# Performance work log

Hardware: AMD Instinct MI355X
Metric: run time of the kernel (lower is better)

The kernel has to match this reference:

```python
import jax, jax.numpy as jnp
import numpy as np

B, S, D, H = 2, 2048, 1024, 16
HD = D // H  # head_dim = 64


def setup_inputs() -> dict:
    key = jax.random.key(0)
    ks = jax.random.split(key, 10)
    sc = 1.0 / np.sqrt(D)
    x = jax.random.normal(ks[0], (B, S, D), dtype=jnp.float32)
    # causal mask, 0 = masked (module does masked_fill(mask == 0, -1e9))
    mask = jnp.broadcast_to(jnp.tril(jnp.ones((S, S), dtype=jnp.int32)), (B, S, S))
    return {
        "x": x,
        "mask": mask,
        "Wq": jax.random.normal(ks[1], (D, D), dtype=jnp.float32) * sc,
        "bq": jnp.zeros((D,), dtype=jnp.float32),
        "Wk": jax.random.normal(ks[2], (D, D), dtype=jnp.float32) * sc,
        "bk": jnp.zeros((D,), dtype=jnp.float32),
        "Wv": jax.random.normal(ks[3], (D, D), dtype=jnp.float32) * sc,
        "bv": jnp.zeros((D,), dtype=jnp.float32),
        "Wo": jax.random.normal(ks[4], (D, D), dtype=jnp.float32) * sc,
        "bo": jnp.zeros((D,), dtype=jnp.float32),
    }


def reference(x, mask, Wq, bq, Wk, bk, Wv, bv, Wo, bo):
    b, s, _ = x.shape
    # torch nn.Linear: y = x @ W.T + b
    def split_heads(t):
        return t.reshape(b, s, H, HD).transpose(0, 2, 1, 3)  # [B,H,S,hd]
    q = split_heads(x @ Wq.T + bq)
    k = split_heads(x @ Wk.T + bk)
    v = split_heads(x @ Wv.T + bv)
    scores = jnp.einsum("bhqd,bhkd->bhqk", q, k) / jnp.sqrt(jnp.float32(HD))
    scores = jnp.where(mask[:, None, :, :] == 0, jnp.float32(-1e9), scores)
    w = jax.nn.softmax(scores, axis=-1)
    out = jnp.einsum("bhqk,bhkd->bhqd", w, v)  # [B,H,S,hd]
    out = out.transpose(0, 2, 1, 3).reshape(b, s, D)
    return out @ Wo.T + bo
```

## Files before the change

kernel.cpp:

```cpp
#include <hip/hip_runtime.h>
#include <cstdint>


typedef __bf16 bf16x8 __attribute__((ext_vector_type(8)));
typedef float f32x4 __attribute__((ext_vector_type(4)));

__device__ inline f32x4 mfma16(bf16x8 a, bf16x8 b, f32x4 c) {
    return __builtin_amdgcn_mfma_f32_16x16x32_bf16(a, b, c, 0, 0, 0);
}

__device__ inline uint16_t f2bf(float f) {
    uint32_t u = __builtin_bit_cast(uint32_t, f);
    u += 0x7FFFu + ((u >> 16) & 1u);
    return (uint16_t)(u >> 16);
}

__device__ inline void gload_lds16(const uint16_t* g, uint16_t* l) {
    __builtin_amdgcn_global_load_lds(
        (const __attribute__((address_space(1))) uint32_t*)g,
        (__attribute__((address_space(3))) uint32_t*)l, 16, 0, 0);
}

__global__ __launch_bounds__(256) void cast_all(const float* __restrict__ x,
                                                const float* __restrict__ wq,
                                                const float* __restrict__ wk,
                                                const float* __restrict__ wv,
                                                const float* __restrict__ wo,
                                                uint16_t* __restrict__ xbf,
                                                uint16_t* __restrict__ wbf) {
    int i = blockIdx.x * 256 + threadIdx.x;
    float4 v;
    uint64_t* dp;
    if (i < (1 << 20)) {
        v = ((const float4*)x)[i];
        dp = (uint64_t*)xbf + i;
    } else {
        int j = i - (1 << 20);
        const float* ws[4] = {wq, wk, wv, wo};
        v = ((const float4*)ws[j >> 18])[j & 0x3FFFF];
        dp = (uint64_t*)wbf + j;
    }
    uint64_t p = (uint64_t)f2bf(v.x) | ((uint64_t)f2bf(v.y) << 16) |
                 ((uint64_t)f2bf(v.z) << 32) | ((uint64_t)f2bf(v.w) << 48);
    *dp = p;
}

template<int OUTF32, int BN>
__global__ __launch_bounds__(256) void gemm128(const uint16_t* __restrict__ A,
                                               const uint16_t* __restrict__ W,
                                               const float* __restrict__ b0,
                                               const float* __restrict__ b1,
                                               const float* __restrict__ b2,
                                               void* __restrict__ o0,
                                               void* __restrict__ o1,
                                               void* __restrict__ o2,
                                               int K, float s0, float s1, float s2) {
    constexpr int NT = BN / 32;
    __shared__ __align__(16) uint16_t SH[2 * (128 + BN) * 32];
    const int tid = threadIdx.x;
    const int lane = tid & 63, w = tid >> 6;
    const int l16 = lane & 15, quad = lane >> 4;
    const int wm = w & 1, wn = w >> 1;
    const int m0 = blockIdx.x * 128, n0 = blockIdx.y * BN;

    f32x4 acc[4][NT] = {};

    const int ci0 = w * 128 + lane;
    const uint16_t* ga0 = A + (size_t)(m0 + (ci0 >> 2)) * K + (ci0 & 3) * 8;
    const int ci1 = ci0 + 64;
    const uint16_t* ga1 = A + (size_t)(m0 + (ci1 >> 2)) * K + (ci1 & 3) * 8;
    const uint16_t* gb0 = W + (size_t)(n0 + (ci0 >> 2)) * K + (ci0 & 3) * 8;
    const uint16_t* gb1 = W + (size_t)(n0 + (ci1 >> 2)) * K + (ci1 & 3) * 8;
    const uint16_t* gbS = W + (size_t)(n0 + (tid >> 2)) * K + (tid & 3) * 8;

    uint16_t* A0 = SH;
    uint16_t* B0 = SH + 128 * 32;
    uint16_t* A1 = SH + (128 + BN) * 32;
    uint16_t* B1 = A1 + 128 * 32;

    gload_lds16(ga0, A0 + (w * 2 + 0) * 512);
    gload_lds16(ga1, A0 + (w * 2 + 1) * 512);
    if constexpr (BN == 128) {
        gload_lds16(gb0, B0 + (w * 2 + 0) * 512);
        gload_lds16(gb1, B0 + (w * 2 + 1) * 512);
    } else {
        gload_lds16(gbS, B0 + w * 512);
    }

    const int niter = K >> 5;
    for (int i = 0; i < niter; ++i) {
        __syncthreads();
        if (i + 1 < niter) {
            const int k1 = (i + 1) << 5;
            uint16_t* Ad = (i & 1) ? A0 : A1;
            uint16_t* Bd = (i & 1) ? B0 : B1;
            gload_lds16(ga0 + k1, Ad + (w * 2 + 0) * 512);
            gload_lds16(ga1 + k1, Ad + (w * 2 + 1) * 512);
            if constexpr (BN == 128) {
                gload_lds16(gb0 + k1, Bd + (w * 2 + 0) * 512);
                gload_lds16(gb1 + k1, Bd + (w * 2 + 1) * 512);
            } else {
                gload_lds16(gbS + k1, Bd + w * 512);
            }
        }
        const uint16_t* Ab = (i & 1) ? A1 : A0;
        const uint16_t* Bb = (i & 1) ? B1 : B0;
        bf16x8 af[4], bw[NT];
#pragma unroll
        for (int t = 0; t < 4; ++t)
            af[t] = *(const bf16x8*)(Ab + (wm * 64 + t * 16 + l16) * 32 + quad * 8);
#pragma unroll
        for (int t = 0; t < NT; ++t)
            bw[t] = *(const bf16x8*)(Bb + (wn * (BN / 2) + t * 16 + l16) * 32 + quad * 8);
#pragma unroll
        for (int mt = 0; mt < 4; ++mt)
#pragma unroll
            for (int nt = 0; nt < NT; ++nt)
                acc[mt][nt] = mfma16(af[mt], bw[nt], acc[mt][nt]);
    }

    const int seg = n0 >> 10, lc0 = n0 & 1023;
    const float* bp = (seg == 0) ? b0 : (seg == 1 ? b1 : b2);
    const float scale = (seg == 0) ? s0 : (seg == 1 ? s1 : s2);
    void* op = (seg == 0) ? o0 : (seg == 1 ? o1 : o2);

    if constexpr (OUTF32) {
#pragma unroll
        for (int nt = 0; nt < NT; ++nt) {
            int lcol = lc0 + wn * (BN / 2) + nt * 16 + l16;
            float bc = bp[lcol];
#pragma unroll
            for (int mt = 0; mt < 4; ++mt)
#pragma unroll
                for (int r = 0; r < 4; ++r) {
                    int row = m0 + wm * 64 + mt * 16 + quad * 4 + r;
                    ((float*)op)[(size_t)row * 1024 + lcol] = (acc[mt][nt][r] + bc) * scale;
                }
        }
    } else {
        __syncthreads();
        uint16_t* EP = SH;
#pragma unroll
        for (int nt = 0; nt < NT; ++nt) {
            float bc = bp[lc0 + wn * (BN / 2) + nt * 16 + l16];
#pragma unroll
            for (int mt = 0; mt < 4; ++mt)
#pragma unroll
                for (int r = 0; r < 4; ++r)
                    EP[(wm * 64 + mt * 16 + quad * 4 + r) * 128 +
                       wn * (BN / 2) + nt * 16 + l16] =
                        f2bf((acc[mt][nt][r] + bc) * scale);
        }
        __syncthreads();
        if (seg == 2) {
            const int bb = m0 >> 11, s0v = m0 & 2047;
            const int h0 = (n0 - 2048) >> 6;
            uint16_t* vtb = (uint16_t*)op + ((size_t)(bb * 16 + h0) * 64) * 2048 + s0v;
#pragma unroll
            for (int it = 0; it < 8; ++it) {
                int id = it * 256 + tid;
                int c = id & 127, sg = id >> 7;
                uint32_t wpk[4];
#pragma unroll
                for (int jj = 0; jj < 4; ++jj) {
                    uint32_t lo = EP[(sg * 8 + 2 * jj) * 128 + c];
                    uint32_t hi = EP[(sg * 8 + 2 * jj + 1) * 128 + c];
                    wpk[jj] = lo | (hi << 16);
                }
                uint4 o; o.x = wpk[0]; o.y = wpk[1]; o.z = wpk[2]; o.w = wpk[3];
                *(uint4*)(vtb + (size_t)c * 2048 + sg * 8) = o;
            }
        } else {
#pragma unroll
            for (int p = 0; p < 8; ++p) {
                int row = p * 16 + (tid >> 4);
                int c8 = (tid & 15) * 8;
                uint4 v = *(const uint4*)(EP + row * 128 + c8);
                *(uint4*)((uint16_t*)op + (size_t)(m0 + row) * 1024 + lc0 + c8) = v;
            }
        }
    }
}

__global__ __launch_bounds__(256) void attn_kernel(const uint16_t* __restrict__ Q,
                                                   const uint16_t* __restrict__ K,
                                                   const uint16_t* __restrict__ Vt,
                                                   uint16_t* __restrict__ att) {
    const int S = 2048, D = 1024;
    constexpr int LD = 72;
    __shared__ __align__(16) uint16_t Plds[4 * 32 * LD];

    const int bh = blockIdx.y;
    const int qb = (bh & 16) ? (int)blockIdx.x : 15 - (int)blockIdx.x;
    const int niter = 2 * qb + 2, kb_diag = 2 * qb;

    const int b = bh >> 4, h = bh & 15;
    const int tid = threadIdx.x, lane = tid & 63, w = tid >> 6;
    const int l16 = lane & 15, quad = lane >> 4;
    const int q0 = qb * 128;
    const size_t baseQK = (size_t)b * S * D + h * 64;
    uint16_t* Pw = Plds + w * (32 * LD);

    bf16x8 aq[2][2];
#pragma unroll
    for (int mt = 0; mt < 2; ++mt)
#pragma unroll
        for (int c = 0; c < 2; ++c)
            aq[mt][c] = *(const bf16x8*)(Q + baseQK +
                (size_t)(q0 + w * 32 + mt * 16 + l16) * D + c * 32 + quad * 8);

    bf16x8 ones;
#pragma unroll
    for (int j = 0; j < 8; ++j) ones[j] = (__bf16)1.0f;

    f32x4 accO[2][4] = {};
    f32x4 accL[2] = {};

    const uint16_t* Kf = K + baseQK + (size_t)l16 * D + quad * 8;
    const uint16_t* Vf = Vt + ((size_t)bh * 64 + l16) * S + quad * 8;

    for (int kb = 0; kb < niter; ++kb) {
        const uint16_t* Kt = Kf + (size_t)(kb * 64) * D;
        bf16x8 k0[4], k1[4];
#pragma unroll
        for (int t = 0; t < 4; ++t) {
            k0[t] = *(const bf16x8*)(Kt + (size_t)(t * 16) * D);
            k1[t] = *(const bf16x8*)(Kt + (size_t)(t * 16) * D + 32);
        }

        f32x4 sc[2][4];
#pragma unroll
        for (int t = 0; t < 4; ++t) {
            f32x4 z0 = {}; f32x4 z1 = {};
            sc[0][t] = mfma16(k1[t], aq[0][1], mfma16(k0[t], aq[0][0], z0));
            sc[1][t] = mfma16(k1[t], aq[1][1], mfma16(k0[t], aq[1][0], z1));
        }

        const uint16_t* Vtt = Vf + kb * 64;
        bf16x8 bv0[4], bv1[4];
#pragma unroll
        for (int nt = 0; nt < 4; ++nt) {
            bv0[nt] = *(const bf16x8*)(Vtt + (size_t)(nt * 16) * S);
            bv1[nt] = *(const bf16x8*)(Vtt + (size_t)(nt * 16) * S + 32);
        }

        if (kb < kb_diag) {
#pragma unroll
            for (int mt = 0; mt < 2; ++mt) {
                uint16_t* prow = Pw + (mt * 16 + l16) * LD + quad * 4;
#pragma unroll
                for (int t = 0; t < 4; ++t) {
                    uint64_t pk = 0;
#pragma unroll
                    for (int r = 0; r < 4; ++r) {
                        float p = __builtin_amdgcn_exp2f(sc[mt][t][r]);
                        pk |= (uint64_t)(uint16_t)(__builtin_bit_cast(uint32_t, p) >> 16)
                              << (16 * r);
                    }
                    *(uint64_t*)(prow + t * 16) = pk;
                }
            }
        } else {
#pragma unroll
            for (int mt = 0; mt < 2; ++mt) {
                const int qrow = q0 + w * 32 + mt * 16 + l16;
                uint16_t* prow = Pw + (mt * 16 + l16) * LD + quad * 4;
#pragma unroll
                for (int t = 0; t < 4; ++t) {
                    const int kc0 = kb * 64 + t * 16 + quad * 4;
                    uint64_t pk = 0;
#pragma unroll
                    for (int r = 0; r < 4; ++r) {
                        float s = sc[mt][t][r];
                        if (kc0 + r > qrow) s = -1e30f;
                        float p = __builtin_amdgcn_exp2f(s);
                        pk |= (uint64_t)(uint16_t)(__builtin_bit_cast(uint32_t, p) >> 16)
                              << (16 * r);
                    }
                    *(uint64_t*)(prow + t * 16) = pk;
                }
            }
        }

        __asm__ volatile("s_waitcnt lgkmcnt(0)" ::: "memory");

        bf16x8 ap0[2], ap1[2];
#pragma unroll
        for (int mt = 0; mt < 2; ++mt) {
            ap0[mt] = *(const bf16x8*)(Pw + (mt * 16 + l16) * LD + quad * 8);
            ap1[mt] = *(const bf16x8*)(Pw + (mt * 16 + l16) * LD + 32 + quad * 8);
        }
#pragma unroll
        for (int nt = 0; nt < 4; ++nt) {
            accO[0][nt] = mfma16(ap1[0], bv1[nt], mfma16(ap0[0], bv0[nt], accO[0][nt]));
            accO[1][nt] = mfma16(ap1[1], bv1[nt], mfma16(ap0[1], bv0[nt], accO[1][nt]));
        }
        accL[0] = mfma16(ap1[0], ones, mfma16(ap0[0], ones, accL[0]));
        accL[1] = mfma16(ap1[1], ones, mfma16(ap0[1], ones, accL[1]));
    }

    __asm__ volatile("s_waitcnt lgkmcnt(0)" ::: "memory");
#pragma unroll
    for (int mt = 0; mt < 2; ++mt)
#pragma unroll
        for (int r = 0; r < 4; ++r) {
            float inv = __builtin_amdgcn_rcpf(accL[mt][r]);
            const int rl = mt * 16 + quad * 4 + r;
#pragma unroll
            for (int nt = 0; nt < 4; ++nt)
                Pw[rl * LD + nt * 16 + l16] = f2bf(accO[mt][nt][r] * inv);
        }
    __asm__ volatile("s_waitcnt lgkmcnt(0)" ::: "memory");
#pragma unroll
    for (int p = 0; p < 4; ++p) {
        int row = p * 8 + (lane >> 3);
        int c8 = (lane & 7) * 8;
        uint4 v = *(const uint4*)(Pw + row * LD + c8);
        *(uint4*)(att + (size_t)(b * S + q0 + w * 32 + row) * 1024 + h * 64 + c8) = v;
    }
}

extern "C" void kernel_launch(void* const* d_in, const int* in_sizes, int n_in,
                              void* d_out, int out_size, void* d_ws, size_t ws_size,
                              hipStream_t stream) {
    const float* x  = (const float*)d_in[0];
    const float* Wq = (const float*)d_in[2];
    const float* bq = (const float*)d_in[3];
    const float* Wk = (const float*)d_in[4];
    const float* bk = (const float*)d_in[5];
    const float* Wv = (const float*)d_in[6];
    const float* bv = (const float*)d_in[7];
    const float* Wo = (const float*)d_in[8];
    const float* bo = (const float*)d_in[9];
    float* out = (float*)d_out;

    const int B = 2, S = 2048, D = 1024, H = 16;
    const int M = B * S;

    uint8_t* w = (uint8_t*)d_ws;
    uint16_t* xbf  = (uint16_t*)(w);
    uint16_t* wqbf = (uint16_t*)(w + (size_t)( 8 << 20));
    uint16_t* qbf  = (uint16_t*)(w + (size_t)(16 << 20));
    uint16_t* kbf  = (uint16_t*)(w + (size_t)(24 << 20));
    uint16_t* vtbf = (uint16_t*)(w + (size_t)(40 << 20));
    uint16_t* wobf = wqbf + (size_t)3 * D * D;
    uint16_t* attbf = xbf;

    cast_all<<<dim3((1 << 21) / 256), dim3(256), 0, stream>>>(
        x, Wq, Wk, Wv, Wo, xbf, wqbf);

    gemm128<0, 128><<<dim3(M / 128, 3072 / 128), dim3(256), 0, stream>>>(
        xbf, wqbf, bq, bk, bv, qbf, kbf, vtbf, D, 0.125f * 1.44269504f, 1.0f, 1.0f);

    attn_kernel<<<dim3(16, B * H), dim3(256), 0, stream>>>(qbf, kbf, vtbf, attbf);

    gemm128<1, 64><<<dim3(M / 128, 1024 / 64), dim3(256), 0, stream>>>(
        attbf, wobf, bo, bo, bo, out, out, out, D, 1.0f, 1.0f, 1.0f);
}
```

Before: 229.2 us.

## Stage K/V tiles in LDS with async double-buffered loads and XOR swizzle

The attention kernel no longer has each wave load its K and V^T fragments straight from global memory. All four waves now load a shared 64x64 K tile and V tile into LDS with global_load_lds, double-buffered so the next tile is prefetched while the current one is computed. An XOR swizzle on the 16-byte chunks avoids LDS bank conflicts on the fragment reads. This cuts redundant global/L2 traffic by sharing tiles across waves, at the cost of a per-iteration block barrier and extra LDS use, which may lower occupancy.

```diff
diff --git a/kernel.cpp b/kernel.cpp
--- a/kernel.cpp
+++ b/kernel.cpp
@@ -187,8 +187,10 @@
                                                    const uint16_t* __restrict__ Vt,
                                                    uint16_t* __restrict__ att) {
     const int S = 2048, D = 1024;
-    constexpr int LD = 72;
-    __shared__ __align__(16) uint16_t Plds[4 * 32 * LD];
+    __shared__ __align__(16) uint16_t Klds[2][64 * 64];
+    __shared__ __align__(16) uint16_t Vlds[2][64 * 64];
+    constexpr int LDP = 72;
+    __shared__ __align__(16) uint16_t Plds[4 * 32 * LDP];
 
     const int bh = blockIdx.y;
     const int qb = (bh & 16) ? (int)blockIdx.x : 15 - (int)blockIdx.x;
@@ -199,7 +201,8 @@
     const int l16 = lane & 15, quad = lane >> 4;
     const int q0 = qb * 128;
     const size_t baseQK = (size_t)b * S * D + h * 64;
-    uint16_t* Pw = Plds + w * (32 * LD);
+    uint16_t* Pw = Plds + w * (32 * LDP);
+    const int sw = l16 & 7;
 
     bf16x8 aq[2][2];
 #pragma unroll
@@ -216,38 +219,60 @@
     f32x4 accO[2][4] = {};
     f32x4 accL[2] = {};
 
-    const uint16_t* Kf = K + baseQK + (size_t)l16 * D + quad * 8;
-    const uint16_t* Vf = Vt + ((size_t)bh * 64 + l16) * S + quad * 8;
+    const int grow = lane >> 3;
+    const int gcol = (lane & 7) ^ grow;
+    const uint16_t* KgL[2];
+    const uint16_t* VgL[2];
+#pragma unroll
+    for (int p = 0; p < 2; ++p) {
+        const int row = 8 * (w * 2 + p) + grow;
+        KgL[p] = K + baseQK + (size_t)row * D + gcol * 8;
+        VgL[p] = Vt + ((size_t)bh * 64 + row) * S + gcol * 8;
+    }
+
+#pragma unroll
+    for (int p = 0; p < 2; ++p) {
+        const int j = w * 2 + p;
+        gload_lds16(KgL[p], (uint16_t*)Klds[0] + j * 512);
+        gload_lds16(VgL[p], (uint16_t*)Vlds[0] + j * 512);
+    }
 
     for (int kb = 0; kb < niter; ++kb) {
-        const uint16_t* Kt = Kf + (size_t)(kb * 64) * D;
-        bf16x8 k0[4], k1[4];
+        __syncthreads();
+        if (kb + 1 < niter) {
+#pragma unroll
+            for (int p = 0; p < 2; ++p) {
+                const int j = w * 2 + p;
+                gload_lds16(KgL[p] + (size_t)(kb + 1) * 64 * D,
+                            (uint16_t*)Klds[(kb + 1) & 1] + j * 512);
+                gload_lds16(VgL[p] + (kb + 1) * 64,
+                            (uint16_t*)Vlds[(kb + 1) & 1] + j * 512);
+            }
+        }
+        const uint16_t* Kb = Klds[kb & 1];
+        const uint16_t* Vb = Vlds[kb & 1];
+
+        f32x4 sc[2][4];
 #pragma unroll
         for (int t = 0; t < 4; ++t) {
-            k0[t] = *(const bf16x8*)(Kt + (size_t)(t * 16) * D);
-            k1[t] = *(const bf16x8*)(Kt + (size_t)(t * 16) * D + 32);
-        }
-
-        f32x4 sc[2][4];
-#pragma unroll
-        for (int t = 0; t < 4; ++t) {
+            bf16x8 bk0 = *(const bf16x8*)(Kb + (t * 16 + l16) * 64 + ((quad ^ sw) << 3));
+            bf16x8 bk1 = *(const bf16x8*)(Kb + (t * 16 + l16) * 64 + (((quad + 4) ^ sw) << 3));
             f32x4 z0 = {}; f32x4 z1 = {};
-            sc[0][t] = mfma16(k1[t], aq[0][1], mfma16(k0[t], aq[0][0], z0));
-            sc[1][t] = mfma16(k1[t], aq[1][1], mfma16(k0[t], aq[1][0], z1));
-        }
-
-        const uint16_t* Vtt = Vf + kb * 64;
+            sc[0][t] = mfma16(bk1, aq[0][1], mfma16(bk0, aq[0][0], z0));
+            sc[1][t] = mfma16(bk1, aq[1][1], mfma16(bk0, aq[1][0], z1));
+        }
+
         bf16x8 bv0[4], bv1[4];
 #pragma unroll
         for (int nt = 0; nt < 4; ++nt) {
-            bv0[nt] = *(const bf16x8*)(Vtt + (size_t)(nt * 16) * S);
-            bv1[nt] = *(const bf16x8*)(Vtt + (size_t)(nt * 16) * S + 32);
+            bv0[nt] = *(const bf16x8*)(Vb + (nt * 16 + l16) * 64 + ((quad ^ sw) << 3));
+            bv1[nt] = *(const bf16x8*)(Vb + (nt * 16 + l16) * 64 + (((quad + 4) ^ sw) << 3));
         }
 
         if (kb < kb_diag) {
 #pragma unroll
             for (int mt = 0; mt < 2; ++mt) {
-                uint16_t* prow = Pw + (mt * 16 + l16) * LD + quad * 4;
+                uint16_t* prow = Pw + (mt * 16 + l16) * LDP + quad * 4;
 #pragma unroll
                 for (int t = 0; t < 4; ++t) {
                     uint64_t pk = 0;
@@ -264,7 +289,7 @@
 #pragma unroll
             for (int mt = 0; mt < 2; ++mt) {
                 const int qrow = q0 + w * 32 + mt * 16 + l16;
-                uint16_t* prow = Pw + (mt * 16 + l16) * LD + quad * 4;
+                uint16_t* prow = Pw + (mt * 16 + l16) * LDP + quad * 4;
 #pragma unroll
                 for (int t = 0; t < 4; ++t) {
                     const int kc0 = kb * 64 + t * 16 + quad * 4;
@@ -287,8 +312,8 @@
         bf16x8 ap0[2], ap1[2];
 #pragma unroll
         for (int mt = 0; mt < 2; ++mt) {
-            ap0[mt] = *(const bf16x8*)(Pw + (mt * 16 + l16) * LD + quad * 8);
-            ap1[mt] = *(const bf16x8*)(Pw + (mt * 16 + l16) * LD + 32 + quad * 8);
+            ap0[mt] = *(const bf16x8*)(Pw + (mt * 16 + l16) * LDP + quad * 8);
+            ap1[mt] = *(const bf16x8*)(Pw + (mt * 16 + l16) * LDP + 32 + quad * 8);
         }
 #pragma unroll
         for (int nt = 0; nt < 4; ++nt) {
@@ -308,14 +333,14 @@
             const int rl = mt * 16 + quad * 4 + r;
 #pragma unroll
             for (int nt = 0; nt < 4; ++nt)
-                Pw[rl * LD + nt * 16 + l16] = f2bf(accO[mt][nt][r] * inv);
+                Pw[rl * LDP + nt * 16 + l16] = f2bf(accO[mt][nt][r] * inv);
         }
     __asm__ volatile("s_waitcnt lgkmcnt(0)" ::: "memory");
 #pragma unroll
     for (int p = 0; p < 4; ++p) {
         int row = p * 8 + (lane >> 3);
         int c8 = (lane & 7) * 8;
-        uint4 v = *(const uint4*)(Pw + row * LD + c8);
+        uint4 v = *(const uint4*)(Pw + row * LDP + c8);
         *(uint4*)(att + (size_t)(b * S + q0 + w * 32 + row) * 1024 + h * 64 + c8) = v;
     }
 }
```

Measured after the change: 201.5 us. 12.1% less time.
